# Kernel tuning notes

Hardware: AMD Instinct MI355X
Metric: run time of the kernel (lower is better)

Reference implementation:

```python
import jax, jax.numpy as jnp
import numpy as np

B, S, H = 16, 8192, 512

def setup_inputs() -> dict:
    key = jax.random.key(0)
    k1, k2, k3, k4, k5 = jax.random.split(key, 5)
    scale = 1.0 / np.sqrt(H)
    return {
        "encoder_outputs": jax.random.normal(k1, (B, S, H), dtype=jnp.float32),
        "query": jax.random.normal(k2, (B, H), dtype=jnp.float32),
        "W_h": jax.random.normal(k3, (H, H), dtype=jnp.float32) * scale,
        "W_q": jax.random.normal(k4, (H, H), dtype=jnp.float32) * scale,
        "v": jax.random.normal(k5, (H,), dtype=jnp.float32) * scale,
    }

def reference(encoder_outputs, query, W_h, W_q, v):
    # h_proj: (B,S,H) = enc @ W_h^T (torch Linear convention)
    h_proj = jnp.einsum('bsh,oh->bso', encoder_outputs, W_h)
    # q_proj: (B,1,H)
    q_proj = jnp.einsum('bh,oh->bo', query, W_q)[:, None, :]
    # scores: (B,S) = tanh(h_proj + q_proj) @ v
    scores = jnp.einsum('bso,o->bs', jnp.tanh(h_proj + q_proj), v)
    alpha = jax.nn.softmax(scores, axis=1)          # (B,S)
    context = jnp.einsum('bs,bsh->bh', alpha, encoder_outputs)  # (B,H)
    return (context, alpha)
```

## Files before the change

kernel.cpp:

```cpp
#include <hip/hip_runtime.h>

typedef float  f32x4  __attribute__((ext_vector_type(4)));
typedef __bf16 bf16x8 __attribute__((ext_vector_type(8)));

#define LOG2E      1.4426950408889634f
#define TWO_LOG2E  2.8853900817779268f

__device__ __forceinline__ float fast_tanh(float x) {
    float e = __builtin_amdgcn_exp2f(x * TWO_LOG2E);
    return 1.0f - 2.0f * __builtin_amdgcn_rcpf(e + 1.0f);
}

__device__ __forceinline__ int a_chunk(int m, int k8) {
    return (((m >> 4) * 16 + (k8 >> 2)) << 6) +
           ((((k8 & 3) << 4) | (m & 15)) ^ ((k8 >> 2) & 7) ^ (((k8 & 3) << 1) & 7));
}

__global__ void wh_swizzle_kernel(const float* __restrict__ Wh,
                                  __bf16* __restrict__ Wswz) {
    int gid = blockIdx.x * 256 + threadIdx.x;
    int n   = gid >> 6;
    int k8  = gid & 63;
    const float* g = Wh + ((long)n << 9) + (k8 << 3);
    f32x4 f0 = *(const f32x4*)g;
    f32x4 f1 = *(const f32x4*)(g + 4);
    bf16x8 val;
    val[0] = (__bf16)f0[0]; val[1] = (__bf16)f0[1];
    val[2] = (__bf16)f0[2]; val[3] = (__bf16)f0[3];
    val[4] = (__bf16)f1[0]; val[5] = (__bf16)f1[1];
    val[6] = (__bf16)f1[2]; val[7] = (__bf16)f1[3];
    int chunk = (((n >> 4) * 16 + (k8 >> 2)) << 6) + (((k8 & 3) << 4) | (n & 15));
    *(bf16x8*)(Wswz + ((long)chunk << 3)) = val;
}

__global__ void qproj_kernel(const float* __restrict__ query,
                             const float* __restrict__ Wq,
                             float* __restrict__ qp) {
    int pair = (blockIdx.x << 2) + (threadIdx.x >> 6);
    int l    = threadIdx.x & 63;
    int b    = pair >> 9;
    long o   = pair & 511;
    const f32x4* q  = (const f32x4*)(query + (b << 9) + (l << 3));
    const f32x4* wr = (const f32x4*)(Wq + (o << 9) + (l << 3));
    f32x4 a0 = q[0], a1 = q[1], w0 = wr[0], w1 = wr[1];
    float acc = a0[0]*w0[0] + a0[1]*w0[1] + a0[2]*w0[2] + a0[3]*w0[3]
              + a1[0]*w1[0] + a1[1]*w1[1] + a1[2]*w1[2] + a1[3]*w1[3];
    #pragma unroll
    for (int off = 1; off < 64; off <<= 1) acc += __shfl_xor(acc, off, 64);
    if (l == 0) qp[pair] = acc;
}

__global__ __launch_bounds__(512, 4) void score_ctx_kernel(
    const float*  __restrict__ enc,
    const __bf16* __restrict__ Wswz,
    const float*  __restrict__ qp,
    const float*  __restrict__ v,
    float* __restrict__ alpha_out,
    float* __restrict__ ctx_acc,
    float* __restrict__ denom)
{
    __shared__ __align__(16) unsigned char ldsA[65536];
    __shared__ float score_lds[512];
    __shared__ float escore[64];

    const int  t    = threadIdx.x;
    const int  w    = t >> 6;
    const int  l    = t & 63;
    const long row0 = (long)blockIdx.x << 6;
    const int  b    = (int)(row0 >> 13);

    f32x4 acc[4][4];
    float vv[4];
    #pragma unroll
    for (int nt = 0; nt < 4; ++nt) {
        int n = (w << 6) + (nt << 4) + (l & 15);
        float q = qp[(b << 9) + n];
        vv[nt] = v[n];
        f32x4 qv = {q, q, q, q};
        #pragma unroll
        for (int mt = 0; mt < 4; ++mt) acc[nt][mt] = qv;
    }

    #pragma unroll
    for (int i = 0; i < 8; ++i) {
        int cflat = t + (i << 9);
        int m = cflat >> 6, k8 = cflat & 63;
        const float* g = enc + ((row0 + m) << 9) + (k8 << 3);
        f32x4 f0 = *(const f32x4*)g;
        f32x4 f1 = *(const f32x4*)(g + 4);
        bf16x8 val;
        val[0] = (__bf16)f0[0]; val[1] = (__bf16)f0[1];
        val[2] = (__bf16)f0[2]; val[3] = (__bf16)f0[3];
        val[4] = (__bf16)f1[0]; val[5] = (__bf16)f1[1];
        val[6] = (__bf16)f1[2]; val[7] = (__bf16)f1[3];
        *(bf16x8*)(ldsA + (a_chunk(m, k8) << 4)) = val;
    }

    __syncthreads();

    const bf16x8* Bg = (const bf16x8*)Wswz;
    #pragma unroll 2
    for (int s = 0; s < 16; ++s) {
        bf16x8 af[4];
        int lowr = l ^ (s & 7) ^ (((l >> 4) << 1) & 7);
        #pragma unroll
        for (int mt = 0; mt < 4; ++mt)
            af[mt] = *(const bf16x8*)(ldsA + (((((mt << 4) + s) << 6) + lowr) << 4));
        #pragma unroll
        for (int nt = 0; nt < 4; ++nt) {
            bf16x8 bf = Bg[((((w << 2) + nt) * 16 + s) << 6) + l];
            #pragma unroll
            for (int mt = 0; mt < 4; ++mt)
                acc[nt][mt] = __builtin_amdgcn_mfma_f32_16x16x32_bf16(
                    af[mt], bf, acc[nt][mt], 0, 0, 0);
        }
    }

    float srow[16];
    #pragma unroll
    for (int i = 0; i < 16; ++i) srow[i] = 0.f;
    #pragma unroll
    for (int nt = 0; nt < 4; ++nt) {
        float vn = vv[nt];
        #pragma unroll
        for (int mt = 0; mt < 4; ++mt)
            #pragma unroll
            for (int r = 0; r < 4; ++r)
                srow[mt * 4 + r] += vn * fast_tanh(acc[nt][mt][r]);
    }
    #pragma unroll
    for (int i = 0; i < 16; ++i) {
        #pragma unroll
        for (int off = 1; off < 16; off <<= 1)
            srow[i] += __shfl_xor(srow[i], off, 64);
    }
    if ((l & 15) == 0) {
        int qd = l >> 4;
        #pragma unroll
        for (int mt = 0; mt < 4; ++mt)
            #pragma unroll
            for (int r = 0; r < 4; ++r)
                score_lds[(w << 6) + (mt << 4) + (qd << 2) + r] = srow[mt * 4 + r];
    }
    __syncthreads();

    if (t < 64) {
        float sc = 0.f;
        #pragma unroll
        for (int ww = 0; ww < 8; ++ww) sc += score_lds[(ww << 6) + t];
        float e = __builtin_amdgcn_exp2f(sc * LOG2E);
        alpha_out[row0 + t] = e;
        escore[t] = e;
        float ssum = e;
        #pragma unroll
        for (int off = 1; off < 64; off <<= 1) ssum += __shfl_xor(ssum, off, 64);
        if (t == 0) atomicAdd(denom + b, ssum);
    }
    __syncthreads();

    float ca[8];
    #pragma unroll
    for (int j = 0; j < 8; ++j) ca[j] = 0.f;
    #pragma unroll
    for (int ii = 0; ii < 8; ++ii) {
        int m = (w << 3) + ii;
        float em = escore[m];
        bf16x8 av = *(const bf16x8*)(ldsA + (a_chunk(m, l) << 4));
        #pragma unroll
        for (int j = 0; j < 8; ++j) ca[j] += em * (float)av[j];
    }
    __syncthreads();
    float* part = (float*)ldsA;
    #pragma unroll
    for (int j = 0; j < 8; ++j) part[t * 9 + j] = ca[j];
    __syncthreads();
    {
        int h = t;
        int k8h = h >> 3, j = h & 7;
        float sum = 0.f;
        #pragma unroll
        for (int rg = 0; rg < 8; ++rg) sum += part[((rg << 6) | k8h) * 9 + j];
        atomicAdd(ctx_acc + ((long)b << 9) + h, sum);
    }
}

__global__ void normalize_kernel(const float* __restrict__ ctx_acc,
                                 const float* __restrict__ denom,
                                 float* __restrict__ out) {
    int i = blockIdx.x * 256 + threadIdx.x;
    if (i < 8192) {
        int b = i >> 9;
        out[i] = ctx_acc[i] / denom[b];
    } else if (i < 8192 + 131072) {
        int b = (i - 8192) >> 13;
        out[i] = out[i] / denom[b];
    }
}

extern "C" void kernel_launch(void* const* d_in, const int* in_sizes, int n_in,
                              void* d_out, int out_size, void* d_ws, size_t ws_size,
                              hipStream_t stream) {
    const float* enc   = (const float*)d_in[0];
    const float* query = (const float*)d_in[1];
    const float* Wh    = (const float*)d_in[2];
    const float* Wq    = (const float*)d_in[3];
    const float* v     = (const float*)d_in[4];
    float* out = (float*)d_out;

    char* ws = (char*)d_ws;
    float*  ctx_acc = (float*)ws;
    float*  denom   = (float*)(ws + 32768);
    float*  qp      = (float*)(ws + 32832);
    __bf16* Wswz    = (__bf16*)(ws + 65600);

    hipMemsetAsync(ws, 0, 32832, stream);
    wh_swizzle_kernel<<<128, 256, 0, stream>>>(Wh, Wswz);
    qproj_kernel<<<2048, 256, 0, stream>>>(query, Wq, qp);
    score_ctx_kernel<<<2048, 512, 0, stream>>>(enc, Wswz, qp, v,
                                               out + 8192, ctx_acc, denom);
    normalize_kernel<<<544, 256, 0, stream>>>(ctx_acc, denom, out);
}
```

Measured before the change: 424.2 us.

## Fuse prolog kernels and pipeline encoder tile staging with MFMA k-steps

Merges the memset, W_h swizzle and q-projection into one prolog kernel to cut launch overhead. In the main kernel, the encoder tile is staged into LDS by K-quarters: the first half is written, then the remaining quarters are loaded and converted while the first MFMA k-steps run, with explicit barriers between phases. This aims to overlap global loads with matrix compute, at the cost of more live registers and hand-placed waitcnt/barrier scheduling.

```diff
diff --git a/kernel.cpp b/kernel.cpp
--- a/kernel.cpp
+++ b/kernel.cpp
@@ -16,38 +16,47 @@
            ((((k8 & 3) << 4) | (m & 15)) ^ ((k8 >> 2) & 7) ^ (((k8 & 3) << 1) & 7));
 }
 
-__global__ void wh_swizzle_kernel(const float* __restrict__ Wh,
-                                  __bf16* __restrict__ Wswz) {
-    int gid = blockIdx.x * 256 + threadIdx.x;
-    int n   = gid >> 6;
-    int k8  = gid & 63;
-    const float* g = Wh + ((long)n << 9) + (k8 << 3);
-    f32x4 f0 = *(const f32x4*)g;
-    f32x4 f1 = *(const f32x4*)(g + 4);
-    bf16x8 val;
-    val[0] = (__bf16)f0[0]; val[1] = (__bf16)f0[1];
-    val[2] = (__bf16)f0[2]; val[3] = (__bf16)f0[3];
-    val[4] = (__bf16)f1[0]; val[5] = (__bf16)f1[1];
-    val[6] = (__bf16)f1[2]; val[7] = (__bf16)f1[3];
-    int chunk = (((n >> 4) * 16 + (k8 >> 2)) << 6) + (((k8 & 3) << 4) | (n & 15));
-    *(bf16x8*)(Wswz + ((long)chunk << 3)) = val;
-}
-
-__global__ void qproj_kernel(const float* __restrict__ query,
-                             const float* __restrict__ Wq,
-                             float* __restrict__ qp) {
-    int pair = (blockIdx.x << 2) + (threadIdx.x >> 6);
-    int l    = threadIdx.x & 63;
-    int b    = pair >> 9;
-    long o   = pair & 511;
-    const f32x4* q  = (const f32x4*)(query + (b << 9) + (l << 3));
-    const f32x4* wr = (const f32x4*)(Wq + (o << 9) + (l << 3));
-    f32x4 a0 = q[0], a1 = q[1], w0 = wr[0], w1 = wr[1];
-    float acc = a0[0]*w0[0] + a0[1]*w0[1] + a0[2]*w0[2] + a0[3]*w0[3]
-              + a1[0]*w1[0] + a1[1]*w1[1] + a1[2]*w1[2] + a1[3]*w1[3];
-    #pragma unroll
-    for (int off = 1; off < 64; off <<= 1) acc += __shfl_xor(acc, off, 64);
-    if (l == 0) qp[pair] = acc;
+__global__ void prolog_kernel(const float* __restrict__ Wh,
+                              __bf16* __restrict__ Wswz,
+                              const float* __restrict__ query,
+                              const float* __restrict__ Wq,
+                              float* __restrict__ qp,
+                              float* __restrict__ ctx_acc,
+                              float* __restrict__ denom) {
+    const int bid = blockIdx.x;
+    const int t   = threadIdx.x;
+    if (bid < 128) {
+        int gid = (bid << 8) + t;
+        int n   = gid >> 6;
+        int k8  = gid & 63;
+        const float* g = Wh + ((long)n << 9) + (k8 << 3);
+        f32x4 f0 = *(const f32x4*)g;
+        f32x4 f1 = *(const f32x4*)(g + 4);
+        bf16x8 val;
+        val[0] = (__bf16)f0[0]; val[1] = (__bf16)f0[1];
+        val[2] = (__bf16)f0[2]; val[3] = (__bf16)f0[3];
+        val[4] = (__bf16)f1[0]; val[5] = (__bf16)f1[1];
+        val[6] = (__bf16)f1[2]; val[7] = (__bf16)f1[3];
+        int chunk = (((n >> 4) * 16 + (k8 >> 2)) << 6) + (((k8 & 3) << 4) | (n & 15));
+        *(bf16x8*)(Wswz + ((long)chunk << 3)) = val;
+    } else if (bid < 2176) {
+        int pair = ((bid - 128) << 2) + (t >> 6);
+        int l    = t & 63;
+        int b    = pair >> 9;
+        long o   = pair & 511;
+        const f32x4* q  = (const f32x4*)(query + (b << 9) + (l << 3));
+        const f32x4* wr = (const f32x4*)(Wq + (o << 9) + (l << 3));
+        f32x4 a0 = q[0], a1 = q[1], w0 = wr[0], w1 = wr[1];
+        float acc = a0[0]*w0[0] + a0[1]*w0[1] + a0[2]*w0[2] + a0[3]*w0[3]
+                  + a1[0]*w1[0] + a1[1]*w1[1] + a1[2]*w1[2] + a1[3]*w1[3];
+        #pragma unroll
+        for (int off = 1; off < 64; off <<= 1) acc += __shfl_xor(acc, off, 64);
+        if (l == 0) qp[pair] = acc;
+    } else {
+        int i = ((bid - 2176) << 8) + t;
+        if (i < 8192)      ctx_acc[i] = 0.f;
+        else if (i < 8208) denom[i - 8192] = 0.f;
+    }
 }
 
 __global__ __launch_bounds__(512, 4) void score_ctx_kernel(
@@ -81,26 +90,35 @@
         for (int mt = 0; mt < 4; ++mt) acc[nt][mt] = qv;
     }
 
-    #pragma unroll
-    for (int i = 0; i < 8; ++i) {
-        int cflat = t + (i << 9);
-        int m = cflat >> 6, k8 = cflat & 63;
-        const float* g = enc + ((row0 + m) << 9) + (k8 << 3);
-        f32x4 f0 = *(const f32x4*)g;
-        f32x4 f1 = *(const f32x4*)(g + 4);
-        bf16x8 val;
-        val[0] = (__bf16)f0[0]; val[1] = (__bf16)f0[1];
-        val[2] = (__bf16)f0[2]; val[3] = (__bf16)f0[3];
-        val[4] = (__bf16)f1[0]; val[5] = (__bf16)f1[1];
-        val[6] = (__bf16)f1[2]; val[7] = (__bf16)f1[3];
-        *(bf16x8*)(ldsA + (a_chunk(m, k8) << 4)) = val;
-    }
-
-    __syncthreads();
+    const int sk8 = t & 15;
+    const int sm  = t >> 4;
+    const float* gbase = enc + ((row0 + sm) << 9);
+
+    auto ld_q = [&](int q8, f32x4* F) {
+        const float* g0 = gbase + (((q8 << 4) | sk8) << 3);
+        F[0] = *(const f32x4*)g0;
+        F[1] = *(const f32x4*)(g0 + 4);
+        const float* g1 = g0 + (32 << 9);
+        F[2] = *(const f32x4*)g1;
+        F[3] = *(const f32x4*)(g1 + 4);
+    };
+    auto wr_q = [&](int q8, f32x4* F) {
+        int k8 = (q8 << 4) | sk8;
+        bf16x8 v0, v1;
+        v0[0] = (__bf16)F[0][0]; v0[1] = (__bf16)F[0][1];
+        v0[2] = (__bf16)F[0][2]; v0[3] = (__bf16)F[0][3];
+        v0[4] = (__bf16)F[1][0]; v0[5] = (__bf16)F[1][1];
+        v0[6] = (__bf16)F[1][2]; v0[7] = (__bf16)F[1][3];
+        v1[0] = (__bf16)F[2][0]; v1[1] = (__bf16)F[2][1];
+        v1[2] = (__bf16)F[2][2]; v1[3] = (__bf16)F[2][3];
+        v1[4] = (__bf16)F[3][0]; v1[5] = (__bf16)F[3][1];
+        v1[6] = (__bf16)F[3][2]; v1[7] = (__bf16)F[3][3];
+        *(bf16x8*)(ldsA + (a_chunk(sm,      k8) << 4)) = v0;
+        *(bf16x8*)(ldsA + (a_chunk(sm + 32, k8) << 4)) = v1;
+    };
 
     const bf16x8* Bg = (const bf16x8*)Wswz;
-    #pragma unroll 2
-    for (int s = 0; s < 16; ++s) {
+    auto kstep = [&](int s) {
         bf16x8 af[4];
         int lowr = l ^ (s & 7) ^ (((l >> 4) << 1) & 7);
         #pragma unroll
@@ -114,7 +132,31 @@
                 acc[nt][mt] = __builtin_amdgcn_mfma_f32_16x16x32_bf16(
                     af[mt], bf, acc[nt][mt], 0, 0, 0);
         }
-    }
+    };
+
+    f32x4 RA[4], RB[4];
+    ld_q(0, RA); ld_q(1, RB);
+    wr_q(0, RA); wr_q(1, RB);
+    ld_q(2, RA);
+
+    asm volatile("s_waitcnt lgkmcnt(0)" ::: "memory");
+    __builtin_amdgcn_s_barrier();
+    __builtin_amdgcn_sched_barrier(0);
+
+    #pragma unroll
+    for (int s = 0; s < 4; ++s) kstep(s);
+    wr_q(2, RA);
+    ld_q(3, RB);
+    #pragma unroll
+    for (int s = 4; s < 8; ++s) kstep(s);
+    wr_q(3, RB);
+
+    asm volatile("s_waitcnt lgkmcnt(0)" ::: "memory");
+    __builtin_amdgcn_s_barrier();
+    __builtin_amdgcn_sched_barrier(0);
+
+    #pragma unroll 2
+    for (int s = 8; s < 16; ++s) kstep(s);
 
     float srow[16];
     #pragma unroll
@@ -213,9 +255,8 @@
     float*  qp      = (float*)(ws + 32832);
     __bf16* Wswz    = (__bf16*)(ws + 65600);
 
-    hipMemsetAsync(ws, 0, 32832, stream);
-    wh_swizzle_kernel<<<128, 256, 0, stream>>>(Wh, Wswz);
-    qproj_kernel<<<2048, 256, 0, stream>>>(query, Wq, qp);
+    prolog_kernel<<<2209, 256, 0, stream>>>(Wh, Wswz, query, Wq, qp,
+                                            ctx_acc, denom);
     score_ctx_kernel<<<2048, 512, 0, stream>>>(enc, Wswz, qp, v,
                                                out + 8192, ctx_acc, denom);
     normalize_kernel<<<544, 256, 0, stream>>>(ctx_acc, denom, out);
```

Measured after the change: 466.3 us. 1.1x slower.

## Fuse prolog kernels with memset and drop LDS reduction syncs in epilogue

Applied to the files above, without the earlier changes.

Combines the W_h swizzle, the query projection and the zeroing of the accumulators into one prolog launch, replacing a memset and two kernels. In the score/context kernel, each wave now reduces the per-row scores and exponentials with shuffles instead of LDS, which removes two block barriers. Each wave also atomically adds its own partial context directly to global memory, dropping the LDS cross-wave reduction. The cost is eight times more global float atomics on the context and denominator accumulators, which may contend heavily on the same addresses.

```diff
diff --git a/kernel.cpp b/kernel.cpp
--- a/kernel.cpp
+++ b/kernel.cpp
@@ -16,38 +16,47 @@
            ((((k8 & 3) << 4) | (m & 15)) ^ ((k8 >> 2) & 7) ^ (((k8 & 3) << 1) & 7));
 }
 
-__global__ void wh_swizzle_kernel(const float* __restrict__ Wh,
-                                  __bf16* __restrict__ Wswz) {
-    int gid = blockIdx.x * 256 + threadIdx.x;
-    int n   = gid >> 6;
-    int k8  = gid & 63;
-    const float* g = Wh + ((long)n << 9) + (k8 << 3);
-    f32x4 f0 = *(const f32x4*)g;
-    f32x4 f1 = *(const f32x4*)(g + 4);
-    bf16x8 val;
-    val[0] = (__bf16)f0[0]; val[1] = (__bf16)f0[1];
-    val[2] = (__bf16)f0[2]; val[3] = (__bf16)f0[3];
-    val[4] = (__bf16)f1[0]; val[5] = (__bf16)f1[1];
-    val[6] = (__bf16)f1[2]; val[7] = (__bf16)f1[3];
-    int chunk = (((n >> 4) * 16 + (k8 >> 2)) << 6) + (((k8 & 3) << 4) | (n & 15));
-    *(bf16x8*)(Wswz + ((long)chunk << 3)) = val;
-}
-
-__global__ void qproj_kernel(const float* __restrict__ query,
-                             const float* __restrict__ Wq,
-                             float* __restrict__ qp) {
-    int pair = (blockIdx.x << 2) + (threadIdx.x >> 6);
-    int l    = threadIdx.x & 63;
-    int b    = pair >> 9;
-    long o   = pair & 511;
-    const f32x4* q  = (const f32x4*)(query + (b << 9) + (l << 3));
-    const f32x4* wr = (const f32x4*)(Wq + (o << 9) + (l << 3));
-    f32x4 a0 = q[0], a1 = q[1], w0 = wr[0], w1 = wr[1];
-    float acc = a0[0]*w0[0] + a0[1]*w0[1] + a0[2]*w0[2] + a0[3]*w0[3]
-              + a1[0]*w1[0] + a1[1]*w1[1] + a1[2]*w1[2] + a1[3]*w1[3];
-    #pragma unroll
-    for (int off = 1; off < 64; off <<= 1) acc += __shfl_xor(acc, off, 64);
-    if (l == 0) qp[pair] = acc;
+__global__ void prolog_kernel(const float* __restrict__ Wh,
+                              __bf16* __restrict__ Wswz,
+                              const float* __restrict__ query,
+                              const float* __restrict__ Wq,
+                              float* __restrict__ qp,
+                              float* __restrict__ ctx_acc,
+                              float* __restrict__ denom) {
+    const int bid = blockIdx.x;
+    const int t   = threadIdx.x;
+    if (bid < 128) {
+        int gid = (bid << 8) + t;
+        int n   = gid >> 6;
+        int k8  = gid & 63;
+        const float* g = Wh + ((long)n << 9) + (k8 << 3);
+        f32x4 f0 = *(const f32x4*)g;
+        f32x4 f1 = *(const f32x4*)(g + 4);
+        bf16x8 val;
+        val[0] = (__bf16)f0[0]; val[1] = (__bf16)f0[1];
+        val[2] = (__bf16)f0[2]; val[3] = (__bf16)f0[3];
+        val[4] = (__bf16)f1[0]; val[5] = (__bf16)f1[1];
+        val[6] = (__bf16)f1[2]; val[7] = (__bf16)f1[3];
+        int chunk = (((n >> 4) * 16 + (k8 >> 2)) << 6) + (((k8 & 3) << 4) | (n & 15));
+        *(bf16x8*)(Wswz + ((long)chunk << 3)) = val;
+    } else if (bid < 2176) {
+        int pair = ((bid - 128) << 2) + (t >> 6);
+        int l    = t & 63;
+        int b    = pair >> 9;
+        long o   = pair & 511;
+        const f32x4* q  = (const f32x4*)(query + (b << 9) + (l << 3));
+        const f32x4* wr = (const f32x4*)(Wq + (o << 9) + (l << 3));
+        f32x4 a0 = q[0], a1 = q[1], w0 = wr[0], w1 = wr[1];
+        float acc = a0[0]*w0[0] + a0[1]*w0[1] + a0[2]*w0[2] + a0[3]*w0[3]
+                  + a1[0]*w1[0] + a1[1]*w1[1] + a1[2]*w1[2] + a1[3]*w1[3];
+        #pragma unroll
+        for (int off = 1; off < 64; off <<= 1) acc += __shfl_xor(acc, off, 64);
+        if (l == 0) qp[pair] = acc;
+    } else {
+        int i = ((bid - 2176) << 8) + t;
+        if (i < 8192)      ctx_acc[i] = 0.f;
+        else if (i < 8208) denom[i - 8192] = 0.f;
+    }
 }
 
 __global__ __launch_bounds__(512, 4) void score_ctx_kernel(
@@ -61,7 +70,6 @@
 {
     __shared__ __align__(16) unsigned char ldsA[65536];
     __shared__ float score_lds[512];
-    __shared__ float escore[64];
 
     const int  t    = threadIdx.x;
     const int  w    = t >> 6;
@@ -144,44 +152,33 @@
     }
     __syncthreads();
 
-    if (t < 64) {
-        float sc = 0.f;
-        #pragma unroll
-        for (int ww = 0; ww < 8; ++ww) sc += score_lds[(ww << 6) + t];
-        float e = __builtin_amdgcn_exp2f(sc * LOG2E);
-        alpha_out[row0 + t] = e;
-        escore[t] = e;
-        float ssum = e;
-        #pragma unroll
-        for (int off = 1; off < 64; off <<= 1) ssum += __shfl_xor(ssum, off, 64);
-        if (t == 0) atomicAdd(denom + b, ssum);
-    }
-    __syncthreads();
+    const int r = t >> 3;
+    float sc = score_lds[((t & 7) << 6) + r];
+    sc += __shfl_xor(sc, 1, 64);
+    sc += __shfl_xor(sc, 2, 64);
+    sc += __shfl_xor(sc, 4, 64);
+    float e = __builtin_amdgcn_exp2f(sc * LOG2E);
+    if ((l & 7) == 0) alpha_out[row0 + r] = e;
+
+    float dsum = e;
+    #pragma unroll
+    for (int off = 1; off < 64; off <<= 1) dsum += __shfl_xor(dsum, off, 64);
+    if (l == 0) atomicAdd(denom + b, dsum * 0.125f);
 
     float ca[8];
     #pragma unroll
     for (int j = 0; j < 8; ++j) ca[j] = 0.f;
     #pragma unroll
     for (int ii = 0; ii < 8; ++ii) {
+        float em = __shfl(e, ii << 3, 64);
         int m = (w << 3) + ii;
-        float em = escore[m];
         bf16x8 av = *(const bf16x8*)(ldsA + (a_chunk(m, l) << 4));
         #pragma unroll
         for (int j = 0; j < 8; ++j) ca[j] += em * (float)av[j];
     }
-    __syncthreads();
-    float* part = (float*)ldsA;
-    #pragma unroll
-    for (int j = 0; j < 8; ++j) part[t * 9 + j] = ca[j];
-    __syncthreads();
-    {
-        int h = t;
-        int k8h = h >> 3, j = h & 7;
-        float sum = 0.f;
-        #pragma unroll
-        for (int rg = 0; rg < 8; ++rg) sum += part[((rg << 6) | k8h) * 9 + j];
-        atomicAdd(ctx_acc + ((long)b << 9) + h, sum);
-    }
+    #pragma unroll
+    for (int j = 0; j < 8; ++j)
+        atomicAdd(ctx_acc + ((long)b << 9) + (l << 3) + j, ca[j]);
 }
 
 __global__ void normalize_kernel(const float* __restrict__ ctx_acc,
@@ -213,9 +210,8 @@
     float*  qp      = (float*)(ws + 32832);
     __bf16* Wswz    = (__bf16*)(ws + 65600);
 
-    hipMemsetAsync(ws, 0, 32832, stream);
-    wh_swizzle_kernel<<<128, 256, 0, stream>>>(Wh, Wswz);
-    qproj_kernel<<<2048, 256, 0, stream>>>(query, Wq, qp);
+    prolog_kernel<<<2209, 256, 0, stream>>>(Wh, Wswz, query, Wq, qp,
+                                            ctx_acc, denom);
     score_ctx_kernel<<<2048, 512, 0, stream>>>(enc, Wswz, qp, v,
                                                out + 8192, ctx_acc, denom);
     normalize_kernel<<<544, 256, 0, stream>>>(ctx_acc, denom, out);
```

After: 1.308 ms. +208.4%, slower.
